# Kernel optimization log

Measured on AMD Instinct MI355X. Metric: run time of the kernel, lower is better.

Reference implementation:

```python
import jax, jax.numpy as jnp
import numpy as np

B, NPER, K = 32, 256, 32
N, E = B * NPER, B * NPER * 32
H, NF, NG, L = 128, 128, 50, 6
CUTOFF = 10.0
LOG2 = 0.6931471805599453


def _ssp(x):
    # ShiftedSoftplus: softplus(x) - log(2)
    return jax.nn.softplus(x) - LOG2


def setup_inputs() -> dict:
    key = jax.random.key(0)
    ks = jax.random.split(key, 16)
    rng = np.random.default_rng(0)

    pos = jnp.asarray(rng.uniform(0.0, 5.0, size=(N, 3)).astype(np.float32))
    z = jnp.asarray(rng.integers(1, 100, size=(N,)).astype(np.int32))
    batch = jnp.asarray((np.arange(N) // NPER).astype(np.int32))
    # K neighbors per atom, within the same graph, no self-loops; dst sorted
    dst = np.repeat(np.arange(N), K)
    off = rng.integers(1, NPER, size=N * K)
    src = (dst % NPER + off) % NPER + (dst // NPER) * NPER
    edge_index = jnp.asarray(np.stack([src, dst]).astype(np.int32))
    domain_ids = jnp.asarray(rng.integers(0, 5, size=(B,)).astype(np.int32))

    def dense(k, i, o):
        return jax.random.normal(k, (i, o), jnp.float32) / np.sqrt(i)

    def stackw(k, i, o):
        return jax.random.normal(k, (L, i, o), jnp.float32) / np.sqrt(i)

    return {
        'pos': pos, 'z': z, 'batch': batch, 'edge_index': edge_index,
        'domain_ids': domain_ids,
        'embedding': jax.random.normal(ks[0], (100, H), jnp.float32),
        'mlp_w1': stackw(ks[1], NG, NF), 'mlp_b1': jnp.zeros((L, NF), jnp.float32),
        'mlp_w2': stackw(ks[2], NF, NF), 'mlp_b2': jnp.zeros((L, NF), jnp.float32),
        'cf_lin1_w': stackw(ks[3], H, NF),
        'cf_lin2_w': stackw(ks[4], NF, H), 'cf_lin2_b': jnp.zeros((L, H), jnp.float32),
        'int_lin_w': stackw(ks[5], H, H), 'int_lin_b': jnp.zeros((L, H), jnp.float32),
        'out_w1': dense(ks[6], H, H // 2), 'out_b1': jnp.zeros((H // 2,), jnp.float32),
        'out_w2': dense(ks[7], H // 2, 1), 'out_b2': jnp.zeros((1,), jnp.float32),
        'dom_emb': jax.random.normal(ks[8], (5, 64), jnp.float32),
        'film_w1': dense(ks[9], 64, 128), 'film_b1': jnp.zeros((128,), jnp.float32),
        'film_w2': dense(ks[10], 128, 128), 'film_b2': jnp.zeros((128,), jnp.float32),
        'gamma_w': dense(ks[11], 128, H), 'gamma_b': jnp.zeros((H,), jnp.float32),
        'beta_w': dense(ks[12], 128, H), 'beta_b': jnp.zeros((H,), jnp.float32),
    }


def reference(pos, z, batch, edge_index, domain_ids, embedding,
              mlp_w1, mlp_b1, mlp_w2, mlp_b2, cf_lin1_w, cf_lin2_w, cf_lin2_b,
              int_lin_w, int_lin_b, out_w1, out_b1, out_w2, out_b2,
              dom_emb, film_w1, film_b1, film_w2, film_b2,
              gamma_w, gamma_b, beta_w, beta_b):
    n_atoms = pos.shape[0]
    n_graphs = domain_ids.shape[0]
    src, dst = edge_index[0], edge_index[1]

    # edge distances, gaussian smearing, cosine cutoff (computed once)
    d = jnp.sqrt(jnp.sum((pos[src] - pos[dst]) ** 2, axis=-1))          # [E]
    offsets = jnp.linspace(0.0, CUTOFF, NG).astype(pos.dtype)
    coeff = -0.5 / (CUTOFF / (NG - 1)) ** 2
    edge_attr = jnp.exp(coeff * (d[:, None] - offsets) ** 2)            # [E,NG]
    C = 0.5 * (jnp.cos(d * (np.pi / CUTOFF)) + 1.0)                     # [E]

    h = embedding[z]                                                    # [N,H]
    for l in range(L):
        # filter network on gaussian basis, modulated by cosine cutoff
        W = (_ssp(edge_attr @ mlp_w1[l] + mlp_b1[l]) @ mlp_w2[l] + mlp_b2[l]) * C[:, None]  # [E,NF]
        x = h @ cf_lin1_w[l]                                            # [N,NF]
        msg = x[src] * W                                                # [E,NF]
        agg = jax.ops.segment_sum(msg, dst, num_segments=n_atoms)       # [N,NF]
        x = agg @ cf_lin2_w[l] + cf_lin2_b[l]                           # [N,H]
        h = h + _ssp(x) @ int_lin_w[l] + int_lin_b[l]                   # residual

    atom_e = _ssp(h @ out_w1 + out_b1) @ out_w2 + out_b2                # [N,1]
    e_graph = jax.ops.segment_sum(atom_e, batch, num_segments=n_graphs) # [B,1]

    # FiLM domain bias (features are zeros, so gamma path contributes 0 - faithful)
    de = dom_emb[domain_ids]                                            # [B,64]
    film = jax.nn.relu(de @ film_w1 + film_b1) @ film_w2 + film_b2      # [B,128]
    gamma = film @ gamma_w + gamma_b                                    # [B,H]
    beta = film @ beta_w + beta_b                                       # [B,H]
    dummy = jnp.zeros((n_graphs, H), pos.dtype)
    bias = jnp.sum(gamma * dummy + beta, axis=-1)                       # [B]

    # faithful broadcast [B,1]+[B] -> [B,B], then sum(dim=1) as in original
    energy = jnp.sum(e_graph + bias[None, :], axis=1)                   # [B]

    forces = jnp.zeros((n_atoms, 3), energy.dtype)
    stress = jnp.zeros((n_graphs, 3, 3), energy.dtype)
    features = jnp.zeros((n_atoms, H), energy.dtype)
    return energy, forces, stress, features
```

## Files before the change

kernel.cpp:

```cpp
#include <hip/hip_runtime.h>
#include <math.h>

using uint = unsigned int;
typedef _Float16 h2    __attribute__((ext_vector_type(2)));
typedef _Float16 f16x8 __attribute__((ext_vector_type(8)));
typedef float    f32x4 __attribute__((ext_vector_type(4)));

#define N_ATOMS 8192
#define NEDGE   262144
#define KNBR    32
#define NGAUSS  50
#define NLAYER  6
#define NB      32
#define GTAB    1024
#define DMAX    8.6603f
#define FCUT    10.0f
#define MB      1048576

#define LSTRIDE 76
#define S_WT    0
#define S_AS    9728
#define S_TS    10944
#define GEMM_SMEM 12160

#define T_W1    0
#define T_W2    4096
#define T_RBF   12288
#define T_HID   13312
#define TAB_SMEM 15360

#define OW1P_OFF 147456
#define M1_OFF   151552
#define M2_OFF   176128
#define WPACK_N  225280

__device__ __forceinline__ float ssp(float x) {
    return fmaxf(x, 0.0f) + log1pf(expf(-fabsf(x))) - 0.69314718055994531f;
}
__device__ __forceinline__ uint pack2(float a, float b) {
    union { h2 h; uint u; } x;
    h2 v; v.x = (_Float16)a; v.y = (_Float16)b; x.h = v; return x.u;
}
__device__ __forceinline__ h2 u2h(uint u) {
    union { uint u; h2 h; } x; x.u = u; return x.h;
}
__device__ __forceinline__ uint h2u(h2 h) {
    union { h2 h; uint u; } x; x.h = h; return x.u;
}
__device__ __forceinline__ float fdot2f(h2 a, h2 b, float c) {
#if __has_builtin(__builtin_amdgcn_fdot2)
    return __builtin_amdgcn_fdot2(a, b, c, false);
#else
    return fmaf((float)a.y, (float)b.y, fmaf((float)a.x, (float)b.x, c));
#endif
}

__device__ __forceinline__ void stage_cp(uint* sm, const uint* __restrict__ src,
                                         int n16, int tid) {
    for (int i = tid; i < n16; i += 256) {
        uint4 v = ((const uint4*)src)[i];
        *(uint4*)&sm[(i >> 4) * LSTRIDE + (i & 15) * 4] = v;
    }
}

template<int NCT>
__device__ __forceinline__ void run_gemm(const uint* sm, int as_off, int lane,
                                         int nb, f32x4* acc) {
    int m = lane & 15, q = lane >> 4;
    #pragma unroll
    for (int ks = 0; ks < 4; ++ks) {
        f16x8 a = *(const f16x8*)&sm[as_off + m * LSTRIDE + q * 4 + ks * 16];
        #pragma unroll
        for (int ct = 0; ct < NCT; ++ct) {
            f16x8 b = *(const f16x8*)&sm[S_WT + (nb + ct * 16 + m) * LSTRIDE + q * 4 + ks * 16];
            acc[ct] = __builtin_amdgcn_mfma_f32_16x16x32_f16(a, b, acc[ct], 0, 0, 0);
        }
    }
}

struct SArgs {
    const float *pos; const int *z; const int *ei; const int *dom;
    const float *emb;
    const float *cf1; const float *cf2w; const float *intw; const float *ow1;
    const float *mw1; const float *mw2;
    const float *dome; const float *fw1; const float *fb1;
    const float *fw2; const float *fb2; const float *bw; const float *bb;
    uint2 *epack; float *h; uint *xA;
    float *gbias; uint *wpack; float *out; int out_size;
};

__global__ void __launch_bounds__(256) k_setup(SArgs a) {
    __shared__ __align__(16) uint sm[S_AS + 1216];
    const int tid = threadIdx.x, bid = blockIdx.x;
    const int gidx = bid * 256 + tid, gsz = 512 * 256;
    const int lane = tid & 63, w = tid >> 6;
    const int m = lane & 15, q = lane >> 4;
    const int rowbase = bid * 16;

    for (int i = gidx; i < a.out_size; i += gsz) a.out[i] = 0.0f;

    for (int idx = gidx; idx < WPACK_N; idx += gsz) {
        if (idx < OW1P_OFF) {
            int mat = idx >> 13, e = idx & 8191;
            int kp = e >> 7, cc = e & 127;
            const float* src = (mat < 6) ? (a.cf1 + mat * 16384)
                            : (mat < 12) ? (a.cf2w + (mat - 6) * 16384)
                                         : (a.intw + (mat - 12) * 16384);
            a.wpack[mat * 8192 + cc * 64 + kp] =
                pack2(src[2 * kp * 128 + cc], src[(2 * kp + 1) * 128 + cc]);
        } else if (idx < M1_OFF) {
            int e = idx - OW1P_OFF;
            int kp = e >> 6, cc = e & 63;
            a.wpack[OW1P_OFF + cc * 64 + kp] =
                pack2(a.ow1[2 * kp * 64 + cc], a.ow1[(2 * kp + 1) * 64 + cc]);
        } else if (idx < M2_OFF) {
            int e = idx - M1_OFF;
            int l = e >> 12, r = e & 4095;
            int kp = r >> 7, cc = r & 127;
            int g0 = 2 * kp;
            float va = (g0 < NGAUSS)     ? a.mw1[l*NGAUSS*128 + g0*128 + cc]     : 0.f;
            float vb = (g0 + 1 < NGAUSS) ? a.mw1[l*NGAUSS*128 + (g0+1)*128 + cc] : 0.f;
            a.wpack[idx] = pack2(va, vb);
        } else {
            int e = idx - M2_OFF;
            int l = e >> 13, r = e & 8191;
            int kp = r >> 7, cc = r & 127;
            a.wpack[idx] = pack2(a.mw2[l*16384 + 2*kp*128 + cc],
                                 a.mw2[l*16384 + (2*kp+1)*128 + cc]);
        }
    }

    const float invdelta = (float)(GTAB - 1) / DMAX;
    #pragma unroll
    for (int t = 0; t < 2; ++t) {
        int e = rowbase * KNBR + t * 256 + tid;
        int s = a.ei[e], d = a.ei[NEDGE + e];
        float dx = a.pos[3*s] - a.pos[3*d];
        float dy = a.pos[3*s+1] - a.pos[3*d+1];
        float dz = a.pos[3*s+2] - a.pos[3*d+2];
        float dist = sqrtf(dx*dx + dy*dy + dz*dz);
        float u = dist * invdelta;
        int i0 = (int)u; i0 = (i0 < GTAB - 2) ? i0 : (GTAB - 2);
        float t2 = u - (float)i0;
        uint tb = pack2(t2, 0.0f) & 0xffffu;
        uint2 ep; ep.x = (uint)s; ep.y = (tb << 16) | (uint)i0;
        a.epack[e] = ep;
    }

    for (int i = tid; i < 1024; i += 256) {
        int r = i >> 6, f2 = i & 63;
        int zz = a.z[rowbase + r];
        float2 v = *(const float2*)&a.emb[zz * 128 + f2 * 2];
        *(float2*)&a.h[(rowbase + r) * 128 + f2 * 2] = v;
        sm[S_AS + r * LSTRIDE + f2] = pack2(v.x, v.y);
    }
    for (int i = tid; i < 2048; i += 256) {
        int m4 = i >> 7, cc = i & 127;
        float v[8];
        #pragma unroll
        for (int j = 0; j < 8; ++j) v[j] = a.cf1[(8 * m4 + j) * 128 + cc];
        uint4 pk; pk.x = pack2(v[0], v[1]); pk.y = pack2(v[2], v[3]);
        pk.z = pack2(v[4], v[5]); pk.w = pack2(v[6], v[7]);
        *(uint4*)&sm[cc * LSTRIDE + m4 * 4] = pk;
    }
    __syncthreads();
    {
        f32x4 acc[2] = {{0,0,0,0},{0,0,0,0}};
        run_gemm<2>(sm, S_AS, lane, w * 32, acc);
        #pragma unroll
        for (int ct = 0; ct < 2; ++ct) {
            int n = w * 32 + ct * 16 + m;
            #pragma unroll
            for (int i = 0; i < 4; ++i) {
                float v = acc[ct][i];
                float u = __shfl_xor(v, 1, 64);
                if (!(lane & 1))
                    a.xA[(rowbase + q * 4 + i) * 64 + (n >> 1)] = pack2(v, u);
            }
        }
    }
    __syncthreads();
    if (bid >= 32 && bid < 64) {
        int g = bid - 32;
        float* fs = (float*)sm;
        if (tid < 64) fs[tid] = a.dome[a.dom[g] * 64 + tid];
        __syncthreads();
        if (tid < 128) {
            float acc = a.fb1[tid];
            for (int i = 0; i < 64; ++i) acc = fmaf(fs[i], a.fw1[i*128 + tid], acc);
            fs[64 + tid] = fmaxf(acc, 0.0f);
        }
        __syncthreads();
        if (tid < 128) {
            float acc = a.fb2[tid];
            for (int i = 0; i < 128; ++i) acc = fmaf(fs[64+i], a.fw2[i*128 + tid], acc);
            fs[192 + tid] = acc;
        }
        __syncthreads();
        if (tid < 128) {
            float acc = a.bb[tid];
            for (int i = 0; i < 128; ++i) acc = fmaf(fs[192+i], a.bw[i*128 + tid], acc);
            #pragma unroll
            for (int off = 32; off > 0; off >>= 1) acc += __shfl_down(acc, off, 64);
            if ((tid & 63) == 0) fs[320 + (tid >> 6)] = acc;
        }
        __syncthreads();
        if (tid == 0) a.gbias[g] = fs[320] + fs[321];
    }
}

__global__ void __launch_bounds__(256) k_table(
    const uint* __restrict__ wpack, const float* __restrict__ mb1,
    const float* __restrict__ mb2, uint* __restrict__ tab2) {
    __shared__ __align__(16) uint sm[TAB_SMEM];
    const int tid = threadIdx.x;
    const int l = blockIdx.x >> 5;
    const int base = (blockIdx.x & 31) * 32;
    { const uint4* s4 = (const uint4*)(wpack + M1_OFF + l*4096);
      uint4* d4 = (uint4*)&sm[T_W1];
      for (int i = tid; i < 1024; i += 256) d4[i] = s4[i]; }
    { const uint4* s4 = (const uint4*)(wpack + M2_OFF + l*8192);
      uint4* d4 = (uint4*)&sm[T_W2];
      for (int i = tid; i < 2048; i += 256) d4[i] = s4[i]; }
    const float delta = DMAX / (float)(GTAB - 1);
    const float gstep = FCUT / (float)(NGAUSS - 1);
    const float coeff = -0.5f / (gstep * gstep);
    for (int i = tid; i < 1024; i += 256) {
        int r = i >> 5, kp = i & 31;
        float dv = (float)(base + r) * delta;
        int g0 = 2 * kp;
        float v0 = 0.f, v1 = 0.f;
        if (g0 < NGAUSS)     { float t = dv - (float)g0 * gstep;     v0 = expf(coeff*t*t); }
        if (g0 + 1 < NGAUSS) { float t = dv - (float)(g0+1) * gstep; v1 = expf(coeff*t*t); }
        sm[T_RBF + i] = pack2(v0, v1);
    }
    __syncthreads();
    int tx = tid & 31, ty = tid >> 5, c0 = tx * 4, tr0 = ty * 4;
    float acc[4][4];
    #pragma unroll
    for (int i = 0; i < 4; ++i) { acc[i][0]=0.f; acc[i][1]=0.f; acc[i][2]=0.f; acc[i][3]=0.f; }
    #pragma unroll
    for (int oct = 0; oct < 8; ++oct) {
        int kp0 = oct * 4;
        uint4 w_[4];
        #pragma unroll
        for (int p = 0; p < 4; ++p) w_[p] = *(const uint4*)&sm[T_W1 + (kp0+p)*128 + c0];
        #pragma unroll
        for (int i = 0; i < 4; ++i) {
            uint4 av = *(const uint4*)&sm[T_RBF + (tr0+i)*32 + kp0];
            uint aa[4] = {av.x, av.y, av.z, av.w};
            #pragma unroll
            for (int p = 0; p < 4; ++p) {
                h2 ap = u2h(aa[p]);
                acc[i][0] = fdot2f(ap, u2h(w_[p].x), acc[i][0]);
                acc[i][1] = fdot2f(ap, u2h(w_[p].y), acc[i][1]);
                acc[i][2] = fdot2f(ap, u2h(w_[p].z), acc[i][2]);
                acc[i][3] = fdot2f(ap, u2h(w_[p].w), acc[i][3]);
            }
        }
    }
    float4 b1v = *(const float4*)&mb1[l*128 + c0];
    #pragma unroll
    for (int i = 0; i < 4; ++i) {
        uint2 o;
        o.x = pack2(ssp(acc[i][0] + b1v.x), ssp(acc[i][1] + b1v.y));
        o.y = pack2(ssp(acc[i][2] + b1v.z), ssp(acc[i][3] + b1v.w));
        *(uint2*)&sm[T_HID + (tr0+i)*64 + (c0 >> 1)] = o;
    }
    __syncthreads();
    float acc2[4][4];
    #pragma unroll
    for (int i = 0; i < 4; ++i) { acc2[i][0]=0.f; acc2[i][1]=0.f; acc2[i][2]=0.f; acc2[i][3]=0.f; }
    #pragma unroll 4
    for (int oct = 0; oct < 16; ++oct) {
        int kp0 = oct * 4;
        uint4 w_[4];
        #pragma unroll
        for (int p = 0; p < 4; ++p) w_[p] = *(const uint4*)&sm[T_W2 + (kp0+p)*128 + c0];
        #pragma unroll
        for (int i = 0; i < 4; ++i) {
            uint4 av = *(const uint4*)&sm[T_HID + (tr0+i)*64 + kp0];
            uint aa[4] = {av.x, av.y, av.z, av.w};
            #pragma unroll
            for (int p = 0; p < 4; ++p) {
                h2 ap = u2h(aa[p]);
                acc2[i][0] = fdot2f(ap, u2h(w_[p].x), acc2[i][0]);
                acc2[i][1] = fdot2f(ap, u2h(w_[p].y), acc2[i][1]);
                acc2[i][2] = fdot2f(ap, u2h(w_[p].z), acc2[i][2]);
                acc2[i][3] = fdot2f(ap, u2h(w_[p].w), acc2[i][3]);
            }
        }
    }
    float4 b2v = *(const float4*)&mb2[l*128 + c0];
    #pragma unroll
    for (int i = 0; i < 4; ++i) {
        int row = base + tr0 + i;
        float dv = (float)row * delta;
        float Cd = 0.5f * (cosf(dv * 0.3141592653589793f) + 1.0f);
        uint2 o;
        o.x = pack2((acc2[i][0] + b2v.x)*Cd, (acc2[i][1] + b2v.y)*Cd);
        o.y = pack2((acc2[i][2] + b2v.z)*Cd, (acc2[i][3] + b2v.w)*Cd);
        *(uint2*)&tab2[(l*GTAB + row)*128 + tx*4] = o;
        if (row > 0)
            *(uint2*)&tab2[(l*GTAB + row - 1)*128 + tx*4 + 2] = o;
    }
}

__global__ void __launch_bounds__(256) k_gather(
    const uint* __restrict__ xin, const uint* __restrict__ tab2l,
    const uint2* __restrict__ epack, uint* __restrict__ agg) {
    const int tid = threadIdx.x;
    const int lane = tid & 63;
    const int atom = blockIdx.x * 4 + (tid >> 6);
    const int side = lane >> 5, l5 = lane & 31;
    uint2 ep = epack[atom * KNBR + l5];
    h2 a0; a0.x = (_Float16)0; a0.y = (_Float16)0;
    h2 a1 = a0;
    #pragma unroll 4
    for (int k = 0; k < 16; ++k) {
        int e = 2 * k + side;
        uint s = __shfl(ep.x, e, 64);
        uint y = __shfl(ep.y, e, 64);
        int i0 = (int)(y & 0xffffu);
        uint th = y >> 16;
        h2 t2 = u2h(th | (th << 16));
        uint4 tv = *(const uint4*)&tab2l[i0 * 128 + l5 * 4];
        uint2 xv = *(const uint2*)&xin[s * 64 + l5 * 2];
        h2 w0 = u2h(tv.x) + t2 * (u2h(tv.z) - u2h(tv.x));
        h2 w1 = u2h(tv.y) + t2 * (u2h(tv.w) - u2h(tv.y));
        a0 = a0 + u2h(xv.x) * w0;
        a1 = a1 + u2h(xv.y) * w1;
    }
    uint u0 = h2u(a0), u1 = h2u(a1);
    uint p0 = __shfl_xor(u0, 32, 64), p1 = __shfl_xor(u1, 32, 64);
    if (side == 0) {
        h2 r0 = u2h(u0) + u2h(p0), r1 = u2h(u1) + u2h(p1);
        uint2 o; o.x = h2u(r0); o.y = h2u(r1);
        *(uint2*)&agg[atom * 64 + l5 * 2] = o;
    }
}

template<bool LAST>
__global__ void __launch_bounds__(256) k_gemmL(
    float* __restrict__ h, const uint* __restrict__ agg, uint* __restrict__ xout,
    const uint* __restrict__ w2p, const uint* __restrict__ w3p,
    const uint* __restrict__ w1np,
    const float* __restrict__ b2, const float* __restrict__ b3,
    const float* __restrict__ ob1, const float* __restrict__ ow2,
    const float* __restrict__ ob2, const float* __restrict__ gbias,
    float* __restrict__ out) {
    __shared__ __align__(16) uint sm[GEMM_SMEM];
    const int tid = threadIdx.x, bid = blockIdx.x;
    const int lane = tid & 63, w = tid >> 6;
    const int m = lane & 15, q = lane >> 4;
    const int rowbase = bid * 16;

    stage_cp(sm, w2p, 2048, tid);
    {   uint4 v = ((const uint4*)(agg + rowbase * 64))[tid];
        *(uint4*)&sm[S_AS + (tid >> 4) * LSTRIDE + (tid & 15) * 4] = v; }
    __syncthreads();
    {
        f32x4 acc[2] = {{0,0,0,0},{0,0,0,0}};
        run_gemm<2>(sm, S_AS, lane, w * 32, acc);
        #pragma unroll
        for (int ct = 0; ct < 2; ++ct) {
            int n = w * 32 + ct * 16 + m;
            float bv = b2[n];
            #pragma unroll
            for (int i = 0; i < 4; ++i) {
                float v = ssp(acc[ct][i] + bv);
                float u = __shfl_xor(v, 1, 64);
                if (!(lane & 1))
                    sm[S_TS + (q * 4 + i) * LSTRIDE + (n >> 1)] = pack2(v, u);
            }
        }
    }
    __syncthreads();
    stage_cp(sm, w3p, 2048, tid);
    __syncthreads();
    {
        f32x4 acc[2] = {{0,0,0,0},{0,0,0,0}};
        run_gemm<2>(sm, S_TS, lane, w * 32, acc);
        #pragma unroll
        for (int ct = 0; ct < 2; ++ct) {
            int n = w * 32 + ct * 16 + m;
            float bv = b3[n];
            #pragma unroll
            for (int i = 0; i < 4; ++i) {
                int r = rowbase + q * 4 + i;
                float hv = h[r * 128 + n] + acc[ct][i] + bv;
                h[r * 128 + n] = hv;
                float u = __shfl_xor(hv, 1, 64);
                if (!(lane & 1))
                    sm[S_AS + (q * 4 + i) * LSTRIDE + (n >> 1)] = pack2(hv, u);
            }
        }
    }
    __syncthreads();
    if (!LAST) {
        stage_cp(sm, w1np, 2048, tid);
        __syncthreads();
        f32x4 acc[2] = {{0,0,0,0},{0,0,0,0}};
        run_gemm<2>(sm, S_AS, lane, w * 32, acc);
        #pragma unroll
        for (int ct = 0; ct < 2; ++ct) {
            int n = w * 32 + ct * 16 + m;
            #pragma unroll
            for (int i = 0; i < 4; ++i) {
                float v = acc[ct][i];
                float u = __shfl_xor(v, 1, 64);
                if (!(lane & 1))
                    xout[(rowbase + q * 4 + i) * 64 + (n >> 1)] = pack2(v, u);
            }
        }
    } else {
        stage_cp(sm, w1np, 1024, tid);
        __syncthreads();
        f32x4 acc[1] = {{0,0,0,0}};
        run_gemm<1>(sm, S_AS, lane, w * 16, acc);
        int n = w * 16 + m;
        float b1v = ob1[n], w2v = ow2[n];
        float part = 0.f;
        #pragma unroll
        for (int i = 0; i < 4; ++i) part += ssp(acc[0][i] + b1v) * w2v;
        #pragma unroll
        for (int mm = 1; mm < 64; mm <<= 1) part += __shfl_xor(part, mm, 64);
        float* fs = (float*)&sm[S_TS];
        if (lane == 0) fs[w] = part;
        __syncthreads();
        if (tid == 0) {
            float bsum = fs[0] + fs[1] + fs[2] + fs[3] + 16.0f * ob2[0];
            float add = 32.0f * bsum;
            if ((bid & 15) == 0) {
                float sb = 0.f;
                for (int j = 0; j < NB; ++j) sb += gbias[j];
                add += sb;
            }
            atomicAdd(&out[bid >> 4], add);
        }
    }
}

extern "C" void kernel_launch(void* const* d_in, const int* in_sizes, int n_in,
                              void* d_out, int out_size, void* d_ws, size_t ws_size,
                              hipStream_t stream) {
    SArgs a;
    a.pos  = (const float*)d_in[0];
    a.z    = (const int*)d_in[1];
    a.ei   = (const int*)d_in[3];
    a.dom  = (const int*)d_in[4];
    a.emb  = (const float*)d_in[5];
    a.mw1  = (const float*)d_in[6];
    const float* mb1 = (const float*)d_in[7];
    a.mw2  = (const float*)d_in[8];
    const float* mb2 = (const float*)d_in[9];
    a.cf1  = (const float*)d_in[10];
    a.cf2w = (const float*)d_in[11];
    const float* cf2b = (const float*)d_in[12];
    a.intw = (const float*)d_in[13];
    const float* intb = (const float*)d_in[14];
    a.ow1  = (const float*)d_in[15];
    const float* ob1  = (const float*)d_in[16];
    const float* ow2  = (const float*)d_in[17];
    const float* ob2  = (const float*)d_in[18];
    a.dome = (const float*)d_in[19];
    a.fw1  = (const float*)d_in[20];
    a.fb1  = (const float*)d_in[21];
    a.fw2  = (const float*)d_in[22];
    a.fb2  = (const float*)d_in[23];
    a.bw   = (const float*)d_in[26];
    a.bb   = (const float*)d_in[27];

    char* ws = (char*)d_ws;
    a.epack   = (uint2*)(ws + 0);
    uint* tab2= (uint*)(ws + 2*MB);
    a.h       = (float*)(ws + 5*MB);
    a.xA      = (uint*)(ws + 9*MB);
    uint* xB  = (uint*)(ws + 11*MB);
    uint* agg = (uint*)(ws + 13*MB);
    a.gbias   = (float*)(ws + 15*MB);
    a.wpack   = (uint*)(ws + 15*MB + 4096);
    a.out = (float*)d_out;
    a.out_size = out_size;

    k_setup<<<512, 256, 0, stream>>>(a);
    k_table<<<192, 256, 0, stream>>>(a.wpack, mb1, mb2, tab2);

    const uint* xr = a.xA;
    uint* xw = xB;
    for (int l = 0; l < NLAYER; ++l) {
        k_gather<<<N_ATOMS/4, 256, 0, stream>>>(xr, tab2 + l*GTAB*128, a.epack, agg);
        const uint* w2p = a.wpack + (6 + l) * 8192;
        const uint* w3p = a.wpack + (12 + l) * 8192;
        if (l < NLAYER - 1) {
            k_gemmL<false><<<512, 256, 0, stream>>>(
                a.h, agg, xw, w2p, w3p, a.wpack + (l + 1) * 8192,
                cf2b + l*128, intb + l*128, ob1, ow2, ob2, a.gbias, a.out);
        } else {
            k_gemmL<true><<<512, 256, 0, stream>>>(
                a.h, agg, xw, w2p, w3p, a.wpack + OW1P_OFF,
                cf2b + l*128, intb + l*128, ob1, ow2, ob2, a.gbias, a.out);
        }
        const uint* tmp = xr; xr = xw; xw = (uint*)tmp;
    }
}
```

Baseline: 277.1 us.

## Fuse per-layer neighbor gather into the layer GEMM kernel via shared memory

The separate gather kernel is removed. Each 16-row GEMM block now computes its own aggregated neighbor features, with each wave handling four atoms, and writes them straight into shared memory instead of round-tripping through a global agg buffer. This drops one launch per layer and the global write and read of the aggregate. In exchange the gather runs with only 512 blocks of 4 waves, each wave doing 4 atoms serially, so the latency-bound gather gets less parallelism and less latency hiding.

Result: faster. 268.9 us (-3.0%).

```diff
diff --git a/kernel.cpp b/kernel.cpp
--- a/kernel.cpp
+++ b/kernel.cpp
@@ -306,43 +306,10 @@
     }
 }
 
-__global__ void __launch_bounds__(256) k_gather(
-    const uint* __restrict__ xin, const uint* __restrict__ tab2l,
-    const uint2* __restrict__ epack, uint* __restrict__ agg) {
-    const int tid = threadIdx.x;
-    const int lane = tid & 63;
-    const int atom = blockIdx.x * 4 + (tid >> 6);
-    const int side = lane >> 5, l5 = lane & 31;
-    uint2 ep = epack[atom * KNBR + l5];
-    h2 a0; a0.x = (_Float16)0; a0.y = (_Float16)0;
-    h2 a1 = a0;
-    #pragma unroll 4
-    for (int k = 0; k < 16; ++k) {
-        int e = 2 * k + side;
-        uint s = __shfl(ep.x, e, 64);
-        uint y = __shfl(ep.y, e, 64);
-        int i0 = (int)(y & 0xffffu);
-        uint th = y >> 16;
-        h2 t2 = u2h(th | (th << 16));
-        uint4 tv = *(const uint4*)&tab2l[i0 * 128 + l5 * 4];
-        uint2 xv = *(const uint2*)&xin[s * 64 + l5 * 2];
-        h2 w0 = u2h(tv.x) + t2 * (u2h(tv.z) - u2h(tv.x));
-        h2 w1 = u2h(tv.y) + t2 * (u2h(tv.w) - u2h(tv.y));
-        a0 = a0 + u2h(xv.x) * w0;
-        a1 = a1 + u2h(xv.y) * w1;
-    }
-    uint u0 = h2u(a0), u1 = h2u(a1);
-    uint p0 = __shfl_xor(u0, 32, 64), p1 = __shfl_xor(u1, 32, 64);
-    if (side == 0) {
-        h2 r0 = u2h(u0) + u2h(p0), r1 = u2h(u1) + u2h(p1);
-        uint2 o; o.x = h2u(r0); o.y = h2u(r1);
-        *(uint2*)&agg[atom * 64 + l5 * 2] = o;
-    }
-}
-
 template<bool LAST>
-__global__ void __launch_bounds__(256) k_gemmL(
-    float* __restrict__ h, const uint* __restrict__ agg, uint* __restrict__ xout,
+__global__ void __launch_bounds__(256) k_layer(
+    float* __restrict__ h, const uint* __restrict__ xin, uint* __restrict__ xout,
+    const uint* __restrict__ tab2l, const uint2* __restrict__ epack,
     const uint* __restrict__ w2p, const uint* __restrict__ w3p,
     const uint* __restrict__ w1np,
     const float* __restrict__ b2, const float* __restrict__ b3,
@@ -356,8 +323,38 @@
     const int rowbase = bid * 16;
 
     stage_cp(sm, w2p, 2048, tid);
-    {   uint4 v = ((const uint4*)(agg + rowbase * 64))[tid];
-        *(uint4*)&sm[S_AS + (tid >> 4) * LSTRIDE + (tid & 15) * 4] = v; }
+    {
+        const int side = lane >> 5, l5 = lane & 31;
+        #pragma unroll
+        for (int p = 0; p < 4; ++p) {
+            int al = p * 4 + w;
+            uint2 ep = epack[(rowbase + al) * KNBR + l5];
+            h2 a0; a0.x = (_Float16)0; a0.y = (_Float16)0;
+            h2 a1 = a0;
+            #pragma unroll 4
+            for (int k = 0; k < 16; ++k) {
+                int e = 2 * k + side;
+                uint s = __shfl(ep.x, e, 64);
+                uint y = __shfl(ep.y, e, 64);
+                int i0 = (int)(y & 0xffffu);
+                uint th = y >> 16;
+                h2 t2 = u2h(th | (th << 16));
+                uint4 tv = *(const uint4*)&tab2l[i0 * 128 + l5 * 4];
+                uint2 xv = *(const uint2*)&xin[s * 64 + l5 * 2];
+                h2 w0 = u2h(tv.x) + t2 * (u2h(tv.z) - u2h(tv.x));
+                h2 w1 = u2h(tv.y) + t2 * (u2h(tv.w) - u2h(tv.y));
+                a0 = a0 + u2h(xv.x) * w0;
+                a1 = a1 + u2h(xv.y) * w1;
+            }
+            uint u0 = h2u(a0), u1 = h2u(a1);
+            uint p0 = __shfl_xor(u0, 32, 64), p1 = __shfl_xor(u1, 32, 64);
+            if (side == 0) {
+                h2 r0 = u2h(u0) + u2h(p0), r1 = u2h(u1) + u2h(p1);
+                uint2 o; o.x = h2u(r0); o.y = h2u(r1);
+                *(uint2*)&sm[S_AS + al * LSTRIDE + l5 * 2] = o;
+            }
+        }
+    }
     __syncthreads();
     {
         f32x4 acc[2] = {{0,0,0,0},{0,0,0,0}};
@@ -477,7 +474,6 @@
     a.h       = (float*)(ws + 5*MB);
     a.xA      = (uint*)(ws + 9*MB);
     uint* xB  = (uint*)(ws + 11*MB);
-    uint* agg = (uint*)(ws + 13*MB);
     a.gbias   = (float*)(ws + 15*MB);
     a.wpack   = (uint*)(ws + 15*MB + 4096);
     a.out = (float*)d_out;
@@ -489,16 +485,17 @@
     const uint* xr = a.xA;
     uint* xw = xB;
     for (int l = 0; l < NLAYER; ++l) {
-        k_gather<<<N_ATOMS/4, 256, 0, stream>>>(xr, tab2 + l*GTAB*128, a.epack, agg);
         const uint* w2p = a.wpack + (6 + l) * 8192;
         const uint* w3p = a.wpack + (12 + l) * 8192;
         if (l < NLAYER - 1) {
-            k_gemmL<false><<<512, 256, 0, stream>>>(
-                a.h, agg, xw, w2p, w3p, a.wpack + (l + 1) * 8192,
+            k_layer<false><<<512, 256, 0, stream>>>(
+                a.h, xr, xw, tab2 + l*GTAB*128, a.epack, w2p, w3p,
+                a.wpack + (l + 1) * 8192,
                 cf2b + l*128, intb + l*128, ob1, ow2, ob2, a.gbias, a.out);
         } else {
-            k_gemmL<true><<<512, 256, 0, stream>>>(
-                a.h, agg, xw, w2p, w3p, a.wpack + OW1P_OFF,
+            k_layer<true><<<512, 256, 0, stream>>>(
+                a.h, xr, xw, tab2 + l*GTAB*128, a.epack, w2p, w3p,
+                a.wpack + OW1P_OFF,
                 cf2b + l*128, intb + l*128, ob1, ow2, ob2, a.gbias, a.out);
         }
         const uint* tmp = xr; xr = xw; xw = (uint*)tmp;
```
